# Performance work log

Measured on AMD Instinct MI355X. Metric: run time of the kernel, lower is better.

The kernel has to match this reference:

```python
import jax, jax.numpy as jnp
import numpy as np

N_NODES = 50000
N_EDGES = 800000
D = 128


def gcn_conv(x, W, b, src, dst, num_nodes):
    """PyG GCNConv: x @ W, add self-loops, symmetric normalization, scatter-add, + bias."""
    x = x @ W  # [N, out]
    loop = jnp.arange(num_nodes, dtype=src.dtype)
    s = jnp.concatenate([src, loop])  # [E+N]
    d = jnp.concatenate([dst, loop])
    w = jnp.ones(s.shape[0], x.dtype)  # edge_weight=None -> ones (self-loop fill=1)
    deg = jax.ops.segment_sum(w, d, num_segments=num_nodes)  # [N]
    dinv = jnp.where(deg > 0, jax.lax.rsqrt(deg), 0.0)
    norm = dinv[s] * dinv[d]  # [E+N]
    out = jax.ops.segment_sum(x[s] * norm[:, None], d, num_segments=num_nodes)
    return out + b


def setup_inputs() -> dict:
    key = jax.random.key(0)
    ks = jax.random.split(key, 8)
    sc = 1.0 / np.sqrt(D)
    x = jax.random.normal(ks[0], (N_NODES, D), dtype=jnp.float32)
    edge_index = jax.random.randint(ks[1], (2, N_EDGES), 0, N_NODES)
    W1 = jax.random.normal(ks[2], (D, D), dtype=jnp.float32) * sc
    W2 = jax.random.normal(ks[3], (D, D), dtype=jnp.float32) * sc
    W3 = jax.random.normal(ks[4], (D, D), dtype=jnp.float32) * sc
    b1 = jnp.zeros((D,), jnp.float32)
    b2 = jnp.zeros((D,), jnp.float32)
    b3 = jnp.zeros((D,), jnp.float32)
    return {"x": x, "edge_index": edge_index, "W1": W1, "b1": b1,
            "W2": W2, "b2": b2, "W3": W3, "b3": b3}


def reference(x, edge_index, W1, b1, W2, b2, W3, b3):
    src, dst = edge_index[0], edge_index[1]
    n = x.shape[0]
    x = jax.nn.relu(gcn_conv(x, W1, b1, src, dst, n))
    x = jax.nn.relu(gcn_conv(x, W2, b2, src, dst, n))
    return gcn_conv(x, W3, b3, src, dst, n)
```

## Files before the change

kernel.cpp:

```cpp
#include <hip/hip_runtime.h>
#include <hip/hip_fp16.h>
#include <math.h>

#define D 128

typedef __attribute__((ext_vector_type(8))) _Float16 half8;
typedef __attribute__((ext_vector_type(4))) float f32x4;


__global__ void count_rank_kernel(const int* __restrict__ dst, int* __restrict__ cnt,
                                  int* __restrict__ rank, int E) {
    int e0 = (blockIdx.x * blockDim.x + threadIdx.x) * 8;
    if (e0 + 7 < E) {
        int4 da = *(const int4*)(dst + e0);
        int4 db = *(const int4*)(dst + e0 + 4);
        int4 ra, rb;
        ra.x = atomicAdd(&cnt[da.x], 1);
        ra.y = atomicAdd(&cnt[da.y], 1);
        ra.z = atomicAdd(&cnt[da.z], 1);
        ra.w = atomicAdd(&cnt[da.w], 1);
        rb.x = atomicAdd(&cnt[db.x], 1);
        rb.y = atomicAdd(&cnt[db.y], 1);
        rb.z = atomicAdd(&cnt[db.z], 1);
        rb.w = atomicAdd(&cnt[db.w], 1);
        *(int4*)(rank + e0)     = ra;
        *(int4*)(rank + e0 + 4) = rb;
    } else {
        for (int e = e0; e < E; ++e) rank[e] = atomicAdd(&cnt[dst[e]], 1);
    }
}

__global__ __launch_bounds__(1024) void scan_kernel(const int* __restrict__ cnt,
                                                    int* __restrict__ rowptr,
                                                    float* __restrict__ dinv,
                                                    int N) {
    __shared__ int wsum[16];
    __shared__ int carry_s;
    int tid  = threadIdx.x;
    int lane = tid & 63;
    int wid  = tid >> 6;
    if (tid == 0) carry_s = 0;
    __syncthreads();
    for (int base = 0; base < N; base += 4096) {
        int i = base + tid * 4;
        int4 v = make_int4(0, 0, 0, 0);
        if (i + 3 < N) v = *(const int4*)(cnt + i);
        else {
            if (i + 0 < N) v.x = cnt[i + 0];
            if (i + 1 < N) v.y = cnt[i + 1];
            if (i + 2 < N) v.z = cnt[i + 2];
            if (i + 3 < N) v.w = cnt[i + 3];
        }
        int s0 = v.x, s1 = s0 + v.y, s2 = s1 + v.z, s3 = s2 + v.w;
        int sc = s3;
        #pragma unroll
        for (int off = 1; off < 64; off <<= 1) {
            int t = __shfl_up(sc, off, 64);
            if (lane >= off) sc += t;
        }
        if (lane == 63) wsum[wid] = sc;
        __syncthreads();
        if (tid < 16) {
            int w = wsum[tid];
            #pragma unroll
            for (int off = 1; off < 16; off <<= 1) {
                int t = __shfl_up(w, off, 64);
                if (tid >= off) w += t;
            }
            wsum[tid] = w;
        }
        __syncthreads();
        int waveoff = (wid > 0) ? wsum[wid - 1] : 0;
        int excl = carry_s + waveoff + (sc - s3);
        if (i + 0 < N) { rowptr[i + 0] = excl;      dinv[i + 0] = rsqrtf((float)v.x + 1.0f); }
        if (i + 1 < N) { rowptr[i + 1] = excl + s0; dinv[i + 1] = rsqrtf((float)v.y + 1.0f); }
        if (i + 2 < N) { rowptr[i + 2] = excl + s1; dinv[i + 2] = rsqrtf((float)v.z + 1.0f); }
        if (i + 3 < N) { rowptr[i + 3] = excl + s2; dinv[i + 3] = rsqrtf((float)v.w + 1.0f); }
        __syncthreads();
        if (tid == 0) carry_s += wsum[15];
        __syncthreads();
    }
    if (tid == 0) rowptr[N] = carry_s;
}

__global__ void fill_kernel(const int* __restrict__ src, const int* __restrict__ dst,
                            const int* __restrict__ rank, const int* __restrict__ rowptr,
                            int* __restrict__ col, int E) {
    int e0 = (blockIdx.x * blockDim.x + threadIdx.x) * 8;
    if (e0 + 7 < E) {
        int4 da = *(const int4*)(dst + e0);
        int4 db = *(const int4*)(dst + e0 + 4);
        int4 ra = *(const int4*)(rank + e0);
        int4 rb = *(const int4*)(rank + e0 + 4);
        int4 sa = *(const int4*)(src + e0);
        int4 sb = *(const int4*)(src + e0 + 4);
        col[rowptr[da.x] + ra.x] = sa.x;
        col[rowptr[da.y] + ra.y] = sa.y;
        col[rowptr[da.z] + ra.z] = sa.z;
        col[rowptr[da.w] + ra.w] = sa.w;
        col[rowptr[db.x] + rb.x] = sb.x;
        col[rowptr[db.y] + rb.y] = sb.y;
        col[rowptr[db.z] + rb.z] = sb.z;
        col[rowptr[db.w] + rb.w] = sb.w;
    } else {
        for (int e = e0; e < E; ++e) col[rowptr[dst[e]] + rank[e]] = src[e];
    }
}


__global__ void convw_kernel(const float* __restrict__ W1, const float* __restrict__ W2,
                             const float* __restrict__ W3, __half* __restrict__ WhT) {
    int i = blockIdx.x * blockDim.x + threadIdx.x;
    int l = i >> 14;
    int j = i & 16383;
    int n = j >> 7, k = j & 127;
    const float* W = (l == 0) ? W1 : (l == 1) ? W2 : W3;
    WhT[(size_t)i] = __float2half(W[(size_t)k * D + n]);
}


__global__ __launch_bounds__(256) void gemm_mfma_f32(const float* __restrict__ X,
                                                     const __half* __restrict__ WhT,
                                                     const float* __restrict__ dinv,
                                                     __half* __restrict__ Y, int M) {
    int tid  = threadIdx.x;
    int wave = tid >> 6;
    int lane = tid & 63;
    int quad = lane >> 4;
    int l16  = lane & 15;
    int m0   = blockIdx.x * 64 + wave * 16;
    if (m0 >= M) return;

    f32x4 acc[8];
    #pragma unroll
    for (int t = 0; t < 8; ++t) acc[t] = (f32x4)0.0f;

    const float* xrow = X + (size_t)(m0 + l16) * D;

    #pragma unroll
    for (int ks = 0; ks < 4; ++ks) {
        int k0 = ks * 32 + quad * 8;
        float4 x0 = *(const float4*)(xrow + k0);
        float4 x1 = *(const float4*)(xrow + k0 + 4);
        half8 a;
        a[0] = (_Float16)x0.x; a[1] = (_Float16)x0.y;
        a[2] = (_Float16)x0.z; a[3] = (_Float16)x0.w;
        a[4] = (_Float16)x1.x; a[5] = (_Float16)x1.y;
        a[6] = (_Float16)x1.z; a[7] = (_Float16)x1.w;
        #pragma unroll
        for (int t = 0; t < 8; ++t) {
            half8 b = *(const half8*)(WhT + (size_t)(t * 16 + l16) * D + k0);
            acc[t] = __builtin_amdgcn_mfma_f32_16x16x32_f16(a, b, acc[t], 0, 0, 0);
        }
    }

    float4 dv = *(const float4*)(dinv + m0 + quad * 4);
    float dvs[4] = {dv.x, dv.y, dv.z, dv.w};
    #pragma unroll
    for (int t = 0; t < 8; ++t) {
        #pragma unroll
        for (int r = 0; r < 4; ++r) {
            int grow = m0 + quad * 4 + r;
            Y[(size_t)grow * D + t * 16 + l16] = __float2half(acc[t][r] * dvs[r]);
        }
    }
}

__global__ __launch_bounds__(256) void gemm_mfma_f16(const __half* __restrict__ Xh,
                                                     const __half* __restrict__ WhT,
                                                     const float* __restrict__ dinv,
                                                     __half* __restrict__ Y, int M) {
    int tid  = threadIdx.x;
    int wave = tid >> 6;
    int lane = tid & 63;
    int quad = lane >> 4;
    int l16  = lane & 15;
    int m0   = blockIdx.x * 64 + wave * 16;
    if (m0 >= M) return;

    f32x4 acc[8];
    #pragma unroll
    for (int t = 0; t < 8; ++t) acc[t] = (f32x4)0.0f;

    const __half* xrow = Xh + (size_t)(m0 + l16) * D;

    #pragma unroll
    for (int ks = 0; ks < 4; ++ks) {
        int k0 = ks * 32 + quad * 8;
        half8 a = *(const half8*)(xrow + k0);
        #pragma unroll
        for (int t = 0; t < 8; ++t) {
            half8 b = *(const half8*)(WhT + (size_t)(t * 16 + l16) * D + k0);
            acc[t] = __builtin_amdgcn_mfma_f32_16x16x32_f16(a, b, acc[t], 0, 0, 0);
        }
    }

    float4 dv = *(const float4*)(dinv + m0 + quad * 4);
    float dvs[4] = {dv.x, dv.y, dv.z, dv.w};
    #pragma unroll
    for (int t = 0; t < 8; ++t) {
        #pragma unroll
        for (int r = 0; r < 4; ++r) {
            int grow = m0 + quad * 4 + r;
            Y[(size_t)grow * D + t * 16 + l16] = __float2half(acc[t][r] * dvs[r]);
        }
    }
}


__device__ __forceinline__ void acc_h8(float2 a[4], half8 v) {
    a[0].x += (float)v[0]; a[0].y += (float)v[1];
    a[1].x += (float)v[2]; a[1].y += (float)v[3];
    a[2].x += (float)v[4]; a[2].y += (float)v[5];
    a[3].x += (float)v[6]; a[3].y += (float)v[7];
}

template <bool FINAL>
__global__ __launch_bounds__(256) void aggregate_kernel(const __half* __restrict__ ys,
                                                        const int* __restrict__ rowptr,
                                                        const int* __restrict__ col,
                                                        const float* __restrict__ dinv,
                                                        const float* __restrict__ b,
                                                        __half* __restrict__ outh,
                                                        float* __restrict__ outf,
                                                        int N) {
    int gwave = (blockIdx.x * blockDim.x + threadIdx.x) >> 6;
    int lane  = threadIdx.x & 63;
    int g     = lane >> 4;
    int l16   = lane & 15;
    if (gwave >= N) return;
    int row = gwave;
    int s = rowptr[row], e = rowptr[row + 1];

    float2 a[4];
    a[0] = a[1] = a[2] = a[3] = make_float2(0.f, 0.f);

    for (int base = s; base < e; base += 64) {
        int idx = base + lane;
        int myc = (idx < e) ? col[idx] : N;
        int nb  = min(64, e - base);
        #pragma unroll 4
        for (int j = 0; j < nb; j += 4) {
            int c = __shfl(myc, j + g);
            half8 v = *(const half8*)(ys + (size_t)c * D + (l16 << 3));
            acc_h8(a, v);
        }
    }

    #pragma unroll
    for (int k = 0; k < 4; ++k) {
        a[k].x += __shfl_xor(a[k].x, 16, 64);
        a[k].y += __shfl_xor(a[k].y, 16, 64);
        a[k].x += __shfl_xor(a[k].x, 32, 64);
        a[k].y += __shfl_xor(a[k].y, 32, 64);
    }

    half8 us = *(const half8*)(ys + (size_t)row * D + (l16 << 3));
    acc_h8(a, us);

    float dv = dinv[row];
    float4 b0 = *(const float4*)(b + (l16 << 3));
    float4 b1 = *(const float4*)(b + (l16 << 3) + 4);
    float r0 = b0.x + dv * a[0].x, r1 = b0.y + dv * a[0].y;
    float r2 = b0.z + dv * a[1].x, r3 = b0.w + dv * a[1].y;
    float r4 = b1.x + dv * a[2].x, r5 = b1.y + dv * a[2].y;
    float r6 = b1.z + dv * a[3].x, r7 = b1.w + dv * a[3].y;

    if (FINAL) {
        if (g == 0)
            *(float4*)(outf + (size_t)row * D + (l16 << 3)) = make_float4(r0, r1, r2, r3);
        else if (g == 1)
            *(float4*)(outf + (size_t)row * D + (l16 << 3) + 4) = make_float4(r4, r5, r6, r7);
    } else {
        if (g == 0) {
            __half2 h0 = __floats2half2_rn(fmaxf(r0, 0.f), fmaxf(r1, 0.f));
            __half2 h1 = __floats2half2_rn(fmaxf(r2, 0.f), fmaxf(r3, 0.f));
            __half2 h2 = __floats2half2_rn(fmaxf(r4, 0.f), fmaxf(r5, 0.f));
            __half2 h3 = __floats2half2_rn(fmaxf(r6, 0.f), fmaxf(r7, 0.f));
            uint4 pk;
            pk.x = *(unsigned int*)&h0; pk.y = *(unsigned int*)&h1;
            pk.z = *(unsigned int*)&h2; pk.w = *(unsigned int*)&h3;
            *(uint4*)(outh + (size_t)row * D + (l16 << 3)) = pk;
        }
    }
}


extern "C" void kernel_launch(void* const* d_in, const int* in_sizes, int n_in,
                              void* d_out, int out_size, void* d_ws, size_t ws_size,
                              hipStream_t stream) {
    const float* x   = (const float*)d_in[0];
    const int*   ei  = (const int*)d_in[1];
    const float* W1  = (const float*)d_in[2];
    const float* b1  = (const float*)d_in[3];
    const float* W2  = (const float*)d_in[4];
    const float* b2  = (const float*)d_in[5];
    const float* W3  = (const float*)d_in[6];
    const float* b3  = (const float*)d_in[7];
    float* out = (float*)d_out;

    const int N = in_sizes[0] / D;
    const int E = in_sizes[1] / 2;
    const int* src = ei;
    const int* dst = ei + E;

    char* ws = (char*)d_ws;
    size_t off = 0;
    auto alloc = [&](size_t bytes) {
        void* p = ws + off;
        off = (off + bytes + 255) & ~(size_t)255;
        return p;
    };
    __half* ys    = (__half*)alloc((size_t)(N + 1) * D * sizeof(__half));
    __half* hs    = (__half*)alloc((size_t)N * D * sizeof(__half));
    int*   cnt    = (int*)alloc((size_t)N * sizeof(int));
    int*   rowptr = (int*)alloc((size_t)(N + 1) * sizeof(int));
    float* dinv   = (float*)alloc((size_t)N * sizeof(float));
    int*   rank   = (int*)alloc((size_t)E * sizeof(int));
    int*   col    = (int*)alloc((size_t)E * sizeof(int));
    __half* WhT   = (__half*)alloc((size_t)3 * D * D * sizeof(__half));
    (void)ws_size; (void)n_in; (void)out_size;

    convw_kernel<<<(3 * D * D + 255) / 256, 256, 0, stream>>>(W1, W2, W3, WhT);

    hipMemsetAsync(cnt, 0, (size_t)N * sizeof(int), stream);
    hipMemsetAsync(ys + (size_t)N * D, 0, (size_t)D * sizeof(__half), stream);
    const int egrid = ((E + 7) / 8 + 255) / 256;
    count_rank_kernel<<<egrid, 256, 0, stream>>>(dst, cnt, rank, E);
    scan_kernel<<<1, 1024, 0, stream>>>(cnt, rowptr, dinv, N);
    fill_kernel<<<egrid, 256, 0, stream>>>(src, dst, rank, rowptr, col, E);

    const int gemm_grid = (N + 63) / 64;
    const int agg_grid  = (N * 64 + 255) / 256;

    gemm_mfma_f32<<<gemm_grid, 256, 0, stream>>>(x, WhT, dinv, ys, N);
    aggregate_kernel<false><<<agg_grid, 256, 0, stream>>>(ys, rowptr, col, dinv, b1, hs, nullptr, N);
    gemm_mfma_f16<<<gemm_grid, 256, 0, stream>>>(hs, WhT + 16384, dinv, ys, N);
    aggregate_kernel<false><<<agg_grid, 256, 0, stream>>>(ys, rowptr, col, dinv, b2, hs, nullptr, N);
    gemm_mfma_f16<<<gemm_grid, 256, 0, stream>>>(hs, WhT + 32768, dinv, ys, N);
    aggregate_kernel<true><<<agg_grid, 256, 0, stream>>>(ys, rowptr, col, dinv, b3, nullptr, out, N);
}
```

Baseline: 340.9 us.

## Fuse neighbor aggregation into next-layer GEMM, drop intermediate hidden buffer

After: 338.0 us. No clear change (-0.8%).

```diff
diff --git a/kernel.cpp b/kernel.cpp
--- a/kernel.cpp
+++ b/kernel.cpp
@@ -166,10 +166,14 @@
     }
 }
 
-__global__ __launch_bounds__(256) void gemm_mfma_f16(const __half* __restrict__ Xh,
-                                                     const __half* __restrict__ WhT,
-                                                     const float* __restrict__ dinv,
-                                                     __half* __restrict__ Y, int M) {
+
+__global__ __launch_bounds__(256) void fused_agg_gemm(const __half* __restrict__ ysin,
+                                                      const int* __restrict__ rowptr,
+                                                      const int* __restrict__ col,
+                                                      const float* __restrict__ dinv,
+                                                      const float* __restrict__ bias,
+                                                      const __half* __restrict__ WhT,
+                                                      __half* __restrict__ ysout, int M) {
     int tid  = threadIdx.x;
     int wave = tid >> 6;
     int lane = tid & 63;
@@ -178,31 +182,88 @@
     int m0   = blockIdx.x * 64 + wave * 16;
     if (m0 >= M) return;
 
-    f32x4 acc[8];
-    #pragma unroll
-    for (int t = 0; t < 8; ++t) acc[t] = (f32x4)0.0f;
-
-    const __half* xrow = Xh + (size_t)(m0 + l16) * D;
-
+    int n = m0 + l16;
+    int s = rowptr[n], e = rowptr[n + 1];
+
+    float acc[4][8];
+    #pragma unroll
+    for (int ks = 0; ks < 4; ++ks)
+        #pragma unroll
+        for (int j = 0; j < 8; ++j) acc[ks][j] = 0.0f;
+
+    const __half* basep = ysin + quad * 8;
+    for (int i = s; i < e; ++i) {
+        int c = col[i];
+        const __half* r = basep + (size_t)c * D;
+        half8 v0 = *(const half8*)(r);
+        half8 v1 = *(const half8*)(r + 32);
+        half8 v2 = *(const half8*)(r + 64);
+        half8 v3 = *(const half8*)(r + 96);
+        #pragma unroll
+        for (int j = 0; j < 8; ++j) {
+            acc[0][j] += (float)v0[j];
+            acc[1][j] += (float)v1[j];
+            acc[2][j] += (float)v2[j];
+            acc[3][j] += (float)v3[j];
+        }
+    }
+    {
+        const __half* r = basep + (size_t)n * D;
+        half8 v0 = *(const half8*)(r);
+        half8 v1 = *(const half8*)(r + 32);
+        half8 v2 = *(const half8*)(r + 64);
+        half8 v3 = *(const half8*)(r + 96);
+        #pragma unroll
+        for (int j = 0; j < 8; ++j) {
+            acc[0][j] += (float)v0[j];
+            acc[1][j] += (float)v1[j];
+            acc[2][j] += (float)v2[j];
+            acc[3][j] += (float)v3[j];
+        }
+    }
+
+    float dv = dinv[n];
+    half8 a[4];
+    #pragma unroll
+    for (int ks = 0; ks < 4; ++ks) {
+        const float* bp = bias + ks * 32 + quad * 8;
+        float4 bq0 = *(const float4*)(bp);
+        float4 bq1 = *(const float4*)(bp + 4);
+        float t0 = fmaxf(bq0.x + dv * acc[ks][0], 0.f);
+        float t1 = fmaxf(bq0.y + dv * acc[ks][1], 0.f);
+        float t2 = fmaxf(bq0.z + dv * acc[ks][2], 0.f);
+        float t3 = fmaxf(bq0.w + dv * acc[ks][3], 0.f);
+        float t4 = fmaxf(bq1.x + dv * acc[ks][4], 0.f);
+        float t5 = fmaxf(bq1.y + dv * acc[ks][5], 0.f);
+        float t6 = fmaxf(bq1.z + dv * acc[ks][6], 0.f);
+        float t7 = fmaxf(bq1.w + dv * acc[ks][7], 0.f);
+        a[ks][0] = (_Float16)t0; a[ks][1] = (_Float16)t1;
+        a[ks][2] = (_Float16)t2; a[ks][3] = (_Float16)t3;
+        a[ks][4] = (_Float16)t4; a[ks][5] = (_Float16)t5;
+        a[ks][6] = (_Float16)t6; a[ks][7] = (_Float16)t7;
+    }
+
+    f32x4 o[8];
+    #pragma unroll
+    for (int t = 0; t < 8; ++t) o[t] = (f32x4)0.0f;
     #pragma unroll
     for (int ks = 0; ks < 4; ++ks) {
         int k0 = ks * 32 + quad * 8;
-        half8 a = *(const half8*)(xrow + k0);
         #pragma unroll
         for (int t = 0; t < 8; ++t) {
             half8 b = *(const half8*)(WhT + (size_t)(t * 16 + l16) * D + k0);
-            acc[t] = __builtin_amdgcn_mfma_f32_16x16x32_f16(a, b, acc[t], 0, 0, 0);
-        }
-    }
-
-    float4 dv = *(const float4*)(dinv + m0 + quad * 4);
-    float dvs[4] = {dv.x, dv.y, dv.z, dv.w};
+            o[t] = __builtin_amdgcn_mfma_f32_16x16x32_f16(a[ks], b, o[t], 0, 0, 0);
+        }
+    }
+
+    float4 dvo = *(const float4*)(dinv + m0 + quad * 4);
+    float dvs[4] = {dvo.x, dvo.y, dvo.z, dvo.w};
     #pragma unroll
     for (int t = 0; t < 8; ++t) {
         #pragma unroll
         for (int r = 0; r < 4; ++r) {
             int grow = m0 + quad * 4 + r;
-            Y[(size_t)grow * D + t * 16 + l16] = __float2half(acc[t][r] * dvs[r]);
+            ysout[(size_t)grow * D + t * 16 + l16] = __float2half(o[t][r] * dvs[r]);
         }
     }
 }
@@ -215,15 +276,13 @@
     a[3].x += (float)v[6]; a[3].y += (float)v[7];
 }
 
-template <bool FINAL>
-__global__ __launch_bounds__(256) void aggregate_kernel(const __half* __restrict__ ys,
-                                                        const int* __restrict__ rowptr,
-                                                        const int* __restrict__ col,
-                                                        const float* __restrict__ dinv,
-                                                        const float* __restrict__ b,
-                                                        __half* __restrict__ outh,
-                                                        float* __restrict__ outf,
-                                                        int N) {
+__global__ __launch_bounds__(256) void aggregate_final(const __half* __restrict__ ys,
+                                                       const int* __restrict__ rowptr,
+                                                       const int* __restrict__ col,
+                                                       const float* __restrict__ dinv,
+                                                       const float* __restrict__ b,
+                                                       float* __restrict__ outf,
+                                                       int N) {
     int gwave = (blockIdx.x * blockDim.x + threadIdx.x) >> 6;
     int lane  = threadIdx.x & 63;
     int g     = lane >> 4;
@@ -237,13 +296,25 @@
 
     for (int base = s; base < e; base += 64) {
         int idx = base + lane;
-        int myc = (idx < e) ? col[idx] : N;
+        int myc = (idx < e) ? col[idx] : 0;
         int nb  = min(64, e - base);
+        int nb4 = nb & ~3;
         #pragma unroll 4
-        for (int j = 0; j < nb; j += 4) {
+        for (int j = 0; j < nb4; j += 4) {
             int c = __shfl(myc, j + g);
             half8 v = *(const half8*)(ys + (size_t)c * D + (l16 << 3));
             acc_h8(a, v);
+        }
+        int rem = nb - nb4;
+        if (rem) {
+            int jj = nb4 + min(g, rem - 1);
+            int c = __shfl(myc, jj);
+            half8 v = *(const half8*)(ys + (size_t)c * D + (l16 << 3));
+            float m = (g < rem) ? 1.f : 0.f;
+            a[0].x += m * (float)v[0]; a[0].y += m * (float)v[1];
+            a[1].x += m * (float)v[2]; a[1].y += m * (float)v[3];
+            a[2].x += m * (float)v[4]; a[2].y += m * (float)v[5];
+            a[3].x += m * (float)v[6]; a[3].y += m * (float)v[7];
         }
     }
 
@@ -266,23 +337,10 @@
     float r4 = b1.x + dv * a[2].x, r5 = b1.y + dv * a[2].y;
     float r6 = b1.z + dv * a[3].x, r7 = b1.w + dv * a[3].y;
 
-    if (FINAL) {
-        if (g == 0)
-            *(float4*)(outf + (size_t)row * D + (l16 << 3)) = make_float4(r0, r1, r2, r3);
-        else if (g == 1)
-            *(float4*)(outf + (size_t)row * D + (l16 << 3) + 4) = make_float4(r4, r5, r6, r7);
-    } else {
-        if (g == 0) {
-            __half2 h0 = __floats2half2_rn(fmaxf(r0, 0.f), fmaxf(r1, 0.f));
-            __half2 h1 = __floats2half2_rn(fmaxf(r2, 0.f), fmaxf(r3, 0.f));
-            __half2 h2 = __floats2half2_rn(fmaxf(r4, 0.f), fmaxf(r5, 0.f));
-            __half2 h3 = __floats2half2_rn(fmaxf(r6, 0.f), fmaxf(r7, 0.f));
-            uint4 pk;
-            pk.x = *(unsigned int*)&h0; pk.y = *(unsigned int*)&h1;
-            pk.z = *(unsigned int*)&h2; pk.w = *(unsigned int*)&h3;
-            *(uint4*)(outh + (size_t)row * D + (l16 << 3)) = pk;
-        }
-    }
+    if (g == 0)
+        *(float4*)(outf + (size_t)row * D + (l16 << 3)) = make_float4(r0, r1, r2, r3);
+    else if (g == 1)
+        *(float4*)(outf + (size_t)row * D + (l16 << 3) + 4) = make_float4(r4, r5, r6, r7);
 }
 
 
@@ -311,8 +369,8 @@
         off = (off + bytes + 255) & ~(size_t)255;
         return p;
     };
-    __half* ys    = (__half*)alloc((size_t)(N + 1) * D * sizeof(__half));
-    __half* hs    = (__half*)alloc((size_t)N * D * sizeof(__half));
+    __half* ysA   = (__half*)alloc((size_t)N * D * sizeof(__half));
+    __half* ysB   = (__half*)alloc((size_t)N * D * sizeof(__half));
     int*   cnt    = (int*)alloc((size_t)N * sizeof(int));
     int*   rowptr = (int*)alloc((size_t)(N + 1) * sizeof(int));
     float* dinv   = (float*)alloc((size_t)N * sizeof(float));
@@ -324,19 +382,16 @@
     convw_kernel<<<(3 * D * D + 255) / 256, 256, 0, stream>>>(W1, W2, W3, WhT);
 
     hipMemsetAsync(cnt, 0, (size_t)N * sizeof(int), stream);
-    hipMemsetAsync(ys + (size_t)N * D, 0, (size_t)D * sizeof(__half), stream);
     const int egrid = ((E + 7) / 8 + 255) / 256;
     count_rank_kernel<<<egrid, 256, 0, stream>>>(dst, cnt, rank, E);
     scan_kernel<<<1, 1024, 0, stream>>>(cnt, rowptr, dinv, N);
     fill_kernel<<<egrid, 256, 0, stream>>>(src, dst, rank, rowptr, col, E);
 
-    const int gemm_grid = (N + 63) / 64;
+    const int tile_grid = (N + 63) / 64;
     const int agg_grid  = (N * 64 + 255) / 256;
 
-    gemm_mfma_f32<<<gemm_grid, 256, 0, stream>>>(x, WhT, dinv, ys, N);
-    aggregate_kernel<false><<<agg_grid, 256, 0, stream>>>(ys, rowptr, col, dinv, b1, hs, nullptr, N);
-    gemm_mfma_f16<<<gemm_grid, 256, 0, stream>>>(hs, WhT + 16384, dinv, ys, N);
-    aggregate_kernel<false><<<agg_grid, 256, 0, stream>>>(ys, rowptr, col, dinv, b2, hs, nullptr, N);
-    gemm_mfma_f16<<<gemm_grid, 256, 0, stream>>>(hs, WhT + 32768, dinv, ys, N);
-    aggregate_kernel<true><<<agg_grid, 256, 0, stream>>>(ys, rowptr, col, dinv, b3, nullptr, out, N);
-}
+    gemm_mfma_f32<<<tile_grid, 256, 0, stream>>>(x, WhT, dinv, ysA, N);
+    fused_agg_gemm<<<tile_grid, 256, 0, stream>>>(ysA, rowptr, col, dinv, b1, WhT + 16384, ysB, N);
+    fused_agg_gemm<<<tile_grid, 256, 0, stream>>>(ysB, rowptr, col, dinv, b2, WhT + 32768, ysA, N);
+    aggregate_final<<<agg_grid, 256, 0, stream>>>(ysA, rowptr, col, dinv, b3, out, N);
+}
```
